# Kernel tuning notes

Hardware: AMD Instinct MI355X
Metric: run time of the kernel (lower is better)

## Reference

```python
import jax, jax.numpy as jnp
import numpy as np

ROUTINGS = 3
EPS = 1e-7  # tf.keras.backend.epsilon()


def _squash(s):
    # s: (B, num_caps, cap_dim)
    n = jnp.linalg.norm(s, axis=-1, keepdims=True)
    return (n ** 2 / (1.0 + n ** 2)) * s / (n + EPS)


def setup_inputs() -> dict:
    key = jax.random.key(0)
    k1, k2 = jax.random.split(key)
    B, N, D_IN, M, C = 64, 2048, 16, 32, 16
    inputs = jax.random.normal(k1, (B, N, D_IN), dtype=jnp.float32)
    # he_normal: std = sqrt(2 / fan_in), fan_in = D_IN for the (1, D_IN, M*C) kernel
    W = jax.random.normal(k2, (D_IN, M, C), dtype=jnp.float32) * np.float32(np.sqrt(2.0 / D_IN))
    return {"inputs": inputs, "W": W}


def reference(inputs, W):
    # prediction vectors u_hat: (B, N, num_caps, cap_dim)
    u_hat = jnp.einsum('bnd,dmc->bnmc', inputs, W)
    b = jnp.zeros(u_hat.shape[:3], dtype=u_hat.dtype)  # (B, N, num_caps)
    v = None
    for _ in range(ROUTINGS):  # fixed small routing count
        c = jax.nn.softmax(b, axis=1)                      # over input capsules
        s = jnp.einsum('bnm,bnmc->bmc', c, u_hat)          # weighted sum
        v = _squash(s)                                     # (B, num_caps, cap_dim)
        b = b + jnp.einsum('bmc,bnmc->bnm', v, u_hat)      # agreement update
    return v
```

## Files before the change

kernel.cpp:

```cpp
#include <hip/hip_runtime.h>
#include <math.h>


#define TPB 512

#define DPP_ADDF(x, ctrl) \
    ((x) + __int_as_float(__builtin_amdgcn_update_dpp( \
        0, __float_as_int(x), (ctrl), 0xF, 0xF, true)))

__global__ __launch_bounds__(TPB, 4)
void capsule_routing_kernel(const float* __restrict__ in,
                            const float* __restrict__ W,
                            float* __restrict__ out)
{
    __shared__ float red[8 * 34];
    __shared__ float fin[34];
    __shared__ float cum[32];
    __shared__ float w_lds[16 * 33];

    const int tid = threadIdx.x;
    const int w   = tid >> 6;
    const int l   = tid & 63;
    const int c4  = l & 3;
    const int b   = blockIdx.x & 63;
    const int m0  = (blockIdx.x >> 6) << 1;

    const float4* __restrict__ inb4 =
        (const float4*)(in + ((size_t)b << 15)) + ((w << 10) + l);

    {
        const int d = tid >> 5, r = tid & 31;
        w_lds[d * 33 + r] = W[(d << 9) + (m0 << 4) + r];
    }
    __syncthreads();

    for (int pass = 0; pass < 3; ++pass) {
        float wv0[4], wv1[4];
        if (pass) {
            #pragma unroll
            for (int j = 0; j < 4; ++j) {
                wv0[j] = cum[(c4 << 2) + j];
                wv1[j] = cum[16 + (c4 << 2) + j];
            }
        }

        float S0 = 0.f, S1 = 0.f;
        float x0[4] = {0.f, 0.f, 0.f, 0.f};
        float x1[4] = {0.f, 0.f, 0.f, 0.f};

        #pragma unroll 4
        for (int g = 0; g < 16; ++g) {
            const float4 f = inb4[g << 6];
            if (pass) {
                float d0 = f.x*wv0[0] + f.y*wv0[1] + f.z*wv0[2] + f.w*wv0[3];
                float d1 = f.x*wv1[0] + f.y*wv1[1] + f.z*wv1[2] + f.w*wv1[3];
                d0 = DPP_ADDF(d0, 0xB1); d0 = DPP_ADDF(d0, 0x4E);
                d1 = DPP_ADDF(d1, 0xB1); d1 = DPP_ADDF(d1, 0x4E);
                const float e0 = __expf(d0);
                const float e1 = __expf(d1);
                S0 += e0; S1 += e1;
                x0[0] += e0*f.x; x0[1] += e0*f.y; x0[2] += e0*f.z; x0[3] += e0*f.w;
                x1[0] += e1*f.x; x1[1] += e1*f.y; x1[2] += e1*f.z; x1[3] += e1*f.w;
            } else {
                x0[0] += f.x; x0[1] += f.y; x0[2] += f.z; x0[3] += f.w;
            }
        }
        if (!pass) {
            #pragma unroll
            for (int j = 0; j < 4; ++j) x1[j] = x0[j];
        }

        float vals[10] = { x0[0], x0[1], x0[2], x0[3],
                           x1[0], x1[1], x1[2], x1[3], S0, S1 };
        #pragma unroll
        for (int v = 0; v < 10; ++v) {
            float x = vals[v];
            x = DPP_ADDF(x, 0x104);
            x = DPP_ADDF(x, 0x108);
            x += __shfl_xor(x, 16);
            x += __shfl_xor(x, 32);
            vals[v] = x;
        }
        if (l < 4) {
            float* rp = &red[w * 34];
            #pragma unroll
            for (int j = 0; j < 4; ++j) {
                rp[1 + (c4 << 2) + j]      = vals[j];
                rp[18 + (c4 << 2) + j]     = vals[4 + j];
            }
            if (l == 0) {
                rp[0]  = pass ? vals[8] : 256.f;
                rp[17] = pass ? vals[9] : 256.f;
            }
        }
        __syncthreads();
        if (tid < 34) {
            float a = 0.f;
            #pragma unroll
            for (int w2 = 0; w2 < 8; ++w2) a += red[w2 * 34 + tid];
            fin[tid] = a;
        }
        __syncthreads();

        if (tid < 32) {
            const int tmi = tid >> 4;
            const int tc  = tid & 15;
            const float rS = 1.f / fin[tmi * 17];
            float s = 0.f;
            #pragma unroll
            for (int d = 0; d < 16; ++d)
                s += fin[tmi * 17 + 1 + d] * w_lds[d * 33 + (tmi << 4) + tc];
            s *= rS;
            float n2 = s * s;
            n2 += __shfl_xor(n2, 1);
            n2 += __shfl_xor(n2, 2);
            n2 += __shfl_xor(n2, 4);
            n2 += __shfl_xor(n2, 8);
            const float nr = sqrtf(n2);
            const float v  = s * (n2 / (1.f + n2)) / (nr + 1e-7f);
            if (pass < 2) {
                float wvv = 0.f;
                #pragma unroll
                for (int c2 = 0; c2 < 16; ++c2)
                    wvv += w_lds[tc * 33 + (tmi << 4) + c2] * __shfl(v, (tmi << 4) + c2);
                if (pass == 0) cum[(tmi << 4) + tc] = wvv;
                else           cum[(tmi << 4) + tc] += wvv;
            } else {
                out[((size_t)b << 9) + ((m0 + tmi) << 4) + tc] = v;
            }
        }
        __syncthreads();
    }
}

extern "C" void kernel_launch(void* const* d_in, const int* in_sizes, int n_in,
                              void* d_out, int out_size, void* d_ws, size_t ws_size,
                              hipStream_t stream) {
    (void)in_sizes; (void)n_in; (void)d_ws; (void)ws_size; (void)out_size;
    const float* in = (const float*)d_in[0];
    const float* W  = (const float*)d_in[1];
    float* out = (float*)d_out;
    hipLaunchKernelGGL(capsule_routing_kernel, dim3(1024), dim3(TPB), 0, stream,
                       in, W, out);
}
```

Before: 83.21 us.

## Process four output capsules per block and use packed float2 math

Each block now handles four output capsules instead of two, so the grid shrinks from 1024 to 512 blocks. Every streamed input vector is reused across twice as many capsules, which halves total input traffic over the three routing passes. The inner dot-product and accumulation loop is rewritten with float2 vectors so the compiler can emit packed FMA instructions. In exchange there is more register pressure (launch bounds relaxed from 4 to 2 blocks per SM) and fewer blocks to fill the GPU, which may reduce latency hiding.

```diff
diff --git a/kernel.cpp b/kernel.cpp
--- a/kernel.cpp
+++ b/kernel.cpp
@@ -4,76 +4,94 @@
 
 #define TPB 512
 
+typedef float vf2 __attribute__((ext_vector_type(2)));
+
 #define DPP_ADDF(x, ctrl) \
     ((x) + __int_as_float(__builtin_amdgcn_update_dpp( \
         0, __float_as_int(x), (ctrl), 0xF, 0xF, true)))
 
-__global__ __launch_bounds__(TPB, 4)
+__global__ __launch_bounds__(TPB, 2)
 void capsule_routing_kernel(const float* __restrict__ in,
                             const float* __restrict__ W,
                             float* __restrict__ out)
 {
-    __shared__ float red[8 * 34];
-    __shared__ float fin[34];
-    __shared__ float cum[32];
-    __shared__ float w_lds[16 * 33];
+    __shared__ float red[8 * 68];
+    __shared__ float fin[68];
+    __shared__ float cum[64];
+    __shared__ float w_lds[16 * 65];
 
     const int tid = threadIdx.x;
     const int w   = tid >> 6;
     const int l   = tid & 63;
     const int c4  = l & 3;
     const int b   = blockIdx.x & 63;
-    const int m0  = (blockIdx.x >> 6) << 1;
+    const int m0  = (blockIdx.x >> 6) << 2;
 
     const float4* __restrict__ inb4 =
         (const float4*)(in + ((size_t)b << 15)) + ((w << 10) + l);
 
-    {
-        const int d = tid >> 5, r = tid & 31;
-        w_lds[d * 33 + r] = W[(d << 9) + (m0 << 4) + r];
+    #pragma unroll
+    for (int k = 0; k < 2; ++k) {
+        const int idx = tid + k * TPB;
+        const int d = idx >> 6, r = idx & 63;
+        w_lds[d * 65 + r] = W[(d << 9) + (m0 << 4) + r];
     }
     __syncthreads();
 
     for (int pass = 0; pass < 3; ++pass) {
-        float wv0[4], wv1[4];
+        vf2 wva[4], wvb[4];
         if (pass) {
+            const float4* cp = (const float4*)cum;
             #pragma unroll
-            for (int j = 0; j < 4; ++j) {
-                wv0[j] = cum[(c4 << 2) + j];
-                wv1[j] = cum[16 + (c4 << 2) + j];
+            for (int m = 0; m < 4; ++m) {
+                const float4 q = cp[(m << 2) + c4];
+                wva[m].x = q.x; wva[m].y = q.y;
+                wvb[m].x = q.z; wvb[m].y = q.w;
             }
         }
 
-        float S0 = 0.f, S1 = 0.f;
-        float x0[4] = {0.f, 0.f, 0.f, 0.f};
-        float x1[4] = {0.f, 0.f, 0.f, 0.f};
+        vf2 xa[4], xb[4];
+        float S[4];
+        #pragma unroll
+        for (int m = 0; m < 4; ++m) {
+            xa[m].x = 0.f; xa[m].y = 0.f;
+            xb[m].x = 0.f; xb[m].y = 0.f;
+            S[m] = 0.f;
+        }
 
-        #pragma unroll 4
+        #pragma unroll 2
         for (int g = 0; g < 16; ++g) {
             const float4 f = inb4[g << 6];
+            vf2 fa, fb;
+            fa.x = f.x; fa.y = f.y; fb.x = f.z; fb.y = f.w;
             if (pass) {
-                float d0 = f.x*wv0[0] + f.y*wv0[1] + f.z*wv0[2] + f.w*wv0[3];
-                float d1 = f.x*wv1[0] + f.y*wv1[1] + f.z*wv1[2] + f.w*wv1[3];
-                d0 = DPP_ADDF(d0, 0xB1); d0 = DPP_ADDF(d0, 0x4E);
-                d1 = DPP_ADDF(d1, 0xB1); d1 = DPP_ADDF(d1, 0x4E);
-                const float e0 = __expf(d0);
-                const float e1 = __expf(d1);
-                S0 += e0; S1 += e1;
-                x0[0] += e0*f.x; x0[1] += e0*f.y; x0[2] += e0*f.z; x0[3] += e0*f.w;
-                x1[0] += e1*f.x; x1[1] += e1*f.y; x1[2] += e1*f.z; x1[3] += e1*f.w;
+                #pragma unroll
+                for (int m = 0; m < 4; ++m) {
+                    vf2 t = fa * wva[m] + fb * wvb[m];
+                    float d = t.x + t.y;
+                    d = DPP_ADDF(d, 0xB1);
+                    d = DPP_ADDF(d, 0x4E);
+                    const float e = __expf(d);
+                    S[m] += e;
+                    xa[m] += fa * e;
+                    xb[m] += fb * e;
+                }
             } else {
-                x0[0] += f.x; x0[1] += f.y; x0[2] += f.z; x0[3] += f.w;
+                xa[0] += fa; xb[0] += fb;
             }
         }
         if (!pass) {
             #pragma unroll
-            for (int j = 0; j < 4; ++j) x1[j] = x0[j];
+            for (int m = 1; m < 4; ++m) { xa[m] = xa[0]; xb[m] = xb[0]; }
         }
 
-        float vals[10] = { x0[0], x0[1], x0[2], x0[3],
-                           x1[0], x1[1], x1[2], x1[3], S0, S1 };
+        float vals[20] = { xa[0].x, xa[0].y, xb[0].x, xb[0].y,
+                           xa[1].x, xa[1].y, xb[1].x, xb[1].y,
+                           xa[2].x, xa[2].y, xb[2].x, xb[2].y,
+                           xa[3].x, xa[3].y, xb[3].x, xb[3].y,
+                           S[0], S[1], S[2], S[3] };
         #pragma unroll
-        for (int v = 0; v < 10; ++v) {
+        for (int v = 0; v < 20; ++v) {
             float x = vals[v];
             x = DPP_ADDF(x, 0x104);
             x = DPP_ADDF(x, 0x108);
@@ -82,34 +100,36 @@
             vals[v] = x;
         }
         if (l < 4) {
-            float* rp = &red[w * 34];
+            float* rp = &red[w * 68];
             #pragma unroll
-            for (int j = 0; j < 4; ++j) {
-                rp[1 + (c4 << 2) + j]      = vals[j];
-                rp[18 + (c4 << 2) + j]     = vals[4 + j];
+            for (int m = 0; m < 4; ++m) {
+                #pragma unroll
+                for (int j = 0; j < 4; ++j)
+                    rp[m * 17 + 1 + (c4 << 2) + j] = vals[(m << 2) + j];
             }
             if (l == 0) {
-                rp[0]  = pass ? vals[8] : 256.f;
-                rp[17] = pass ? vals[9] : 256.f;
+                #pragma unroll
+                for (int m = 0; m < 4; ++m)
+                    rp[m * 17] = pass ? vals[16 + m] : 256.f;
             }
         }
         __syncthreads();
-        if (tid < 34) {
+        if (tid < 68) {
             float a = 0.f;
             #pragma unroll
-            for (int w2 = 0; w2 < 8; ++w2) a += red[w2 * 34 + tid];
+            for (int w2 = 0; w2 < 8; ++w2) a += red[w2 * 68 + tid];
             fin[tid] = a;
         }
         __syncthreads();
 
-        if (tid < 32) {
+        if (tid < 64) {
             const int tmi = tid >> 4;
             const int tc  = tid & 15;
             const float rS = 1.f / fin[tmi * 17];
             float s = 0.f;
             #pragma unroll
             for (int d = 0; d < 16; ++d)
-                s += fin[tmi * 17 + 1 + d] * w_lds[d * 33 + (tmi << 4) + tc];
+                s += fin[tmi * 17 + 1 + d] * w_lds[d * 65 + (tmi << 4) + tc];
             s *= rS;
             float n2 = s * s;
             n2 += __shfl_xor(n2, 1);
@@ -122,7 +142,7 @@
                 float wvv = 0.f;
                 #pragma unroll
                 for (int c2 = 0; c2 < 16; ++c2)
-                    wvv += w_lds[tc * 33 + (tmi << 4) + c2] * __shfl(v, (tmi << 4) + c2);
+                    wvv += w_lds[tc * 65 + (tmi << 4) + c2] * __shfl(v, (tmi << 4) + c2);
                 if (pass == 0) cum[(tmi << 4) + tc] = wvv;
                 else           cum[(tmi << 4) + tc] += wvv;
             } else {
@@ -140,6 +160,6 @@
     const float* in = (const float*)d_in[0];
     const float* W  = (const float*)d_in[1];
     float* out = (float*)d_out;
-    hipLaunchKernelGGL(capsule_routing_kernel, dim3(1024), dim3(TPB), 0, stream,
+    hipLaunchKernelGGL(capsule_routing_kernel, dim3(512), dim3(TPB), 0, stream,
                        in, W, out);
 }
```

After: 81.37 us. 1.02x faster.
